# Kernel tuning notes

Hardware: AMD Instinct MI355X
Metric: run time of the kernel (lower is better)

Reference implementation:

```python
import jax, jax.numpy as jnp
import numpy as np

RANK = 8
ALPHA = 16.0
SCALING = ALPHA / RANK  # LoRA scaling alpha/rank
B, T, P, C = 8, 16, 197, 1024


def setup_inputs() -> dict:
    key = jax.random.key(0)
    k = jax.random.split(key, 8)
    hidden_states = jax.random.normal(k[0], (B, T, P, C), jnp.float32)
    frame_mask = jnp.ones((B, T), jnp.float32)
    # kaiming_uniform_(a=sqrt(5)) on an (out,in) Linear -> U(-1/sqrt(in), 1/sqrt(in))
    s_down = 1.0 / np.sqrt(C).astype(np.float32)
    down_w = jax.random.uniform(k[1], (RANK, C), jnp.float32, -s_down, s_down)
    # PyTorch LSTM default init: U(-1/sqrt(hidden), 1/sqrt(hidden)) for all params
    s_l = 1.0 / np.sqrt(RANK).astype(np.float32)
    w_ih = jax.random.uniform(k[2], (4 * RANK, RANK), jnp.float32, -s_l, s_l)
    w_hh = jax.random.uniform(k[3], (4 * RANK, RANK), jnp.float32, -s_l, s_l)
    b_ih = jax.random.uniform(k[4], (4 * RANK,), jnp.float32, -s_l, s_l)
    b_hh = jax.random.uniform(k[5], (4 * RANK,), jnp.float32, -s_l, s_l)
    # original zero-inits up; use small random so the reference output is non-trivial
    up_w = jax.random.normal(k[6], (C, RANK), jnp.float32) * 0.02
    return {
        "hidden_states": hidden_states,
        "num_frames": T,
        "frame_mask": frame_mask,
        "down_w": down_w,
        "w_ih": w_ih,
        "w_hh": w_hh,
        "b_ih": b_ih,
        "b_hh": b_hh,
        "up_w": up_w,
    }


def _lstm(x, w_ih, w_hh, b_ih, b_hh):
    """Single-layer unidirectional LSTM, PyTorch gate order (i,f,g,o).
    x: (T, N, R) time-major. Returns all hidden states (T, N, R)."""
    n, r = x.shape[1], w_hh.shape[1]
    bias = b_ih + b_hh

    def step(carry, x_t):
        h, c = carry
        gates = x_t @ w_ih.T + h @ w_hh.T + bias  # (N, 4R)
        i, f, g, o = jnp.split(gates, 4, axis=-1)
        c = jax.nn.sigmoid(f) * c + jax.nn.sigmoid(i) * jnp.tanh(g)
        h = jax.nn.sigmoid(o) * jnp.tanh(c)
        return (h, c), h

    init = (jnp.zeros((n, r), x.dtype), jnp.zeros((n, r), x.dtype))
    _, hs = jax.lax.scan(step, init, x)
    return hs


def reference(hidden_states, num_frames, frame_mask, down_w, w_ih, w_hh, b_ih, b_hh, up_w):
    b, t, p, c = hidden_states.shape
    assert t == num_frames
    # LoRA down: (B,T,P,C) x (R,C) -> (B,T,P,R)  (dropout is identity in eval)
    red = jnp.einsum('btpc,rc->btpr', hidden_states, down_w)
    red = red * frame_mask[:, :, None, None]
    # temporal LSTM over T, batch = B*P, in rank space
    seq = red.transpose(1, 0, 2, 3).reshape(t, b * p, -1)  # (T, B*P, R)
    hs = _lstm(seq, w_ih, w_hh, b_ih, b_hh)                # (T, B*P, R)
    out = hs.reshape(t, b, p, -1).transpose(1, 0, 2, 3)    # (B, T, P, R)
    out = out * frame_mask[:, :, None, None]
    # LoRA up + scaling: (B,T,P,R) x (C,R) -> (B,T,P,C)
    delta = jnp.einsum('btpr,or->btpo', out, up_w) * SCALING
    return delta
```

## Files before the change

kernel.cpp:

```cpp
#include <hip/hip_runtime.h>
#include <math.h>

#define BB 8
#define TT 16
#define PP 197
#define CC 1024
#define RR 8
#define NROWS (BB * TT * PP)
#define NPAIRS (NROWS / 2)
#define NSEQ  (BB * PP)
#define LORA_SCALE 2.0f

__device__ __forceinline__ float sigf(float x) {
    x = fminf(fmaxf(x, -30.f), 30.f);
    return 1.0f / (1.0f + __expf(-x));
}
__device__ __forceinline__ float tanh_fast(float x) {
    x = fminf(fmaxf(x, -15.f), 15.f);
    float e = __expf(-2.0f * x);
    return (1.0f - e) / (1.0f + e);
}
__device__ __forceinline__ float dot4(const float4& a, const float4& b) {
    return a.x * b.x + a.y * b.y + a.z * b.z + a.w * b.w;
}

__global__ __launch_bounds__(256) void k_down(const float* __restrict__ hs,
                                              const float* __restrict__ dw,
                                              const float* __restrict__ fm,
                                              float* __restrict__ red) {
    const int lane = threadIdx.x & 63;
    const int wid  = (blockIdx.x * blockDim.x + threadIdx.x) >> 6;
    const int nw   = (gridDim.x * blockDim.x) >> 6;

    float4 w[RR][4];
#pragma unroll
    for (int r = 0; r < RR; ++r)
#pragma unroll
        for (int k = 0; k < 4; ++k)
            w[r][k] = *(const float4*)(dw + r * CC + k * 256 + lane * 4);

    for (int pr = wid; pr < NPAIRS; pr += nw) {
        const int row0 = pr * 2;
        float4 xa[4], xb[4];
        const float* rpa = hs + (size_t)row0 * CC;
        const float* rpb = rpa + CC;
#pragma unroll
        for (int k = 0; k < 4; ++k) xa[k] = *(const float4*)(rpa + k * 256 + lane * 4);
#pragma unroll
        for (int k = 0; k < 4; ++k) xb[k] = *(const float4*)(rpb + k * 256 + lane * 4);

        float acca[RR], accb[RR];
#pragma unroll
        for (int r = 0; r < RR; ++r) {
            float a = 0.f, b = 0.f;
#pragma unroll
            for (int k = 0; k < 4; ++k) {
                a += dot4(xa[k], w[r][k]);
                b += dot4(xb[k], w[r][k]);
            }
            acca[r] = a; accb[r] = b;
        }
#pragma unroll
        for (int d = 32; d >= 1; d >>= 1) {
#pragma unroll
            for (int r = 0; r < RR; ++r) {
                acca[r] += __shfl_xor(acca[r], d, 64);
                accb[r] += __shfl_xor(accb[r], d, 64);
            }
        }
        if (lane == 0) {
            const float ma = fm[row0 / PP];
            const float mb = fm[(row0 + 1) / PP];
            float4* opa = (float4*)(red + (size_t)row0 * RR);
            opa[0] = make_float4(acca[0] * ma, acca[1] * ma, acca[2] * ma, acca[3] * ma);
            opa[1] = make_float4(acca[4] * ma, acca[5] * ma, acca[6] * ma, acca[7] * ma);
            opa[2] = make_float4(accb[0] * mb, accb[1] * mb, accb[2] * mb, accb[3] * mb);
            opa[3] = make_float4(accb[4] * mb, accb[5] * mb, accb[6] * mb, accb[7] * mb);
        }
    }
}

__global__ __launch_bounds__(64) void k_lstm(const float* __restrict__ red,
                                             const float* __restrict__ fm,
                                             const float* __restrict__ w_ih,
                                             const float* __restrict__ w_hh,
                                             const float* __restrict__ b_ih,
                                             const float* __restrict__ b_hh,
                                             float* __restrict__ hsm) {
    const int tid = blockIdx.x * blockDim.x + threadIdx.x;
    const int n = tid >> 3;
    const int r = tid & 7;
    const int lane = threadIdx.x & 63;
    const int grp = lane & 56;
    if (n >= NSEQ) return;

    float wi_i[8], wi_f[8], wi_g[8], wi_o[8];
    float wh_i[8], wh_f[8], wh_g[8], wh_o[8];
#pragma unroll
    for (int j = 0; j < 8; ++j) {
        wi_i[j] = w_ih[(r) * 8 + j];
        wi_f[j] = w_ih[(8 + r) * 8 + j];
        wi_g[j] = w_ih[(16 + r) * 8 + j];
        wi_o[j] = w_ih[(24 + r) * 8 + j];
        wh_i[j] = w_hh[(r) * 8 + j];
        wh_f[j] = w_hh[(8 + r) * 8 + j];
        wh_g[j] = w_hh[(16 + r) * 8 + j];
        wh_o[j] = w_hh[(24 + r) * 8 + j];
    }
    const float bi = b_ih[r] + b_hh[r];
    const float bf = b_ih[8 + r] + b_hh[8 + r];
    const float bg = b_ih[16 + r] + b_hh[16 + r];
    const float bo = b_ih[24 + r] + b_hh[24 + r];

    const int b = n / PP, p = n - (n / PP) * PP;
    const size_t base = ((size_t)b * TT * PP + p) * RR + r;
    const size_t tstride = (size_t)PP * RR;

    float xs[TT], msk[TT];
#pragma unroll
    for (int t = 0; t < TT; ++t) xs[t] = red[base + (size_t)t * tstride];
#pragma unroll
    for (int t = 0; t < TT; ++t) msk[t] = fm[b * TT + t];

    float h = 0.f, c = 0.f;
#pragma unroll
    for (int t = 0; t < TT; ++t) {
        float gi = bi, gf = bf, gg = bg, go = bo;
#pragma unroll
        for (int j = 0; j < 8; ++j) {
            const float xv = __shfl(xs[t], grp + j, 64);
            const float hv = __shfl(h, grp + j, 64);
            gi += wi_i[j] * xv + wh_i[j] * hv;
            gf += wi_f[j] * xv + wh_f[j] * hv;
            gg += wi_g[j] * xv + wh_g[j] * hv;
            go += wi_o[j] * xv + wh_o[j] * hv;
        }
        c = sigf(gf) * c + sigf(gi) * tanh_fast(gg);
        h = sigf(go) * tanh_fast(c);
        hsm[base + (size_t)t * tstride] = h * msk[t];
    }
}

__global__ __launch_bounds__(256) void k_up(const float* __restrict__ hsm,
                                            const float* __restrict__ up,
                                            float* __restrict__ out) {
    const int lane = threadIdx.x & 63;
    const int wid  = (blockIdx.x * blockDim.x + threadIdx.x) >> 6;
    const int nw   = (gridDim.x * blockDim.x) >> 6;

    float4 u0[16], u1[16];
#pragma unroll
    for (int g = 0; g < 16; ++g) {
        const float* pp = up + (size_t)(g * 64 + lane) * RR;
        u0[g] = *(const float4*)(pp);
        u1[g] = *(const float4*)(pp + 4);
    }

    for (int row = wid; row < NROWS; row += nw) {
        const float* hp = hsm + (size_t)row * RR;
        float4 h0 = *(const float4*)(hp);
        float4 h1 = *(const float4*)(hp + 4);
        h0.x *= LORA_SCALE; h0.y *= LORA_SCALE; h0.z *= LORA_SCALE; h0.w *= LORA_SCALE;
        h1.x *= LORA_SCALE; h1.y *= LORA_SCALE; h1.z *= LORA_SCALE; h1.w *= LORA_SCALE;
        float* op = out + (size_t)row * CC + lane;
#pragma unroll
        for (int g = 0; g < 16; ++g) {
            op[g * 64] = dot4(h0, u0[g]) + dot4(h1, u1[g]);
        }
    }
}

extern "C" void kernel_launch(void* const* d_in, const int* in_sizes, int n_in,
                              void* d_out, int out_size, void* d_ws, size_t ws_size,
                              hipStream_t stream) {
    const float* hs  = (const float*)d_in[0];
    const float* fm  = (const float*)d_in[2];
    const float* dw  = (const float*)d_in[3];
    const float* wih = (const float*)d_in[4];
    const float* whh = (const float*)d_in[5];
    const float* bih = (const float*)d_in[6];
    const float* bhh = (const float*)d_in[7];
    const float* up  = (const float*)d_in[8];
    float* out = (float*)d_out;

    float* red = (float*)d_ws;
    float* hsm = red + (size_t)NROWS * RR;

    k_down<<<512, 256, 0, stream>>>(hs, dw, fm, red);
    k_lstm<<<197, 64, 0, stream>>>(red, fm, wih, whh, bih, bhh, hsm);
    k_up<<<512, 256, 0, stream>>>(hsm, up, out);
}
```

Before: 210.6 us.

## Software-pipeline row loads in down/up kernels and double grid size

The down-projection kernel now handles one row per iteration and prefetches the next row's hidden states while computing the current one, replacing the previous two-rows-per-iteration batching. The up-projection kernel likewise prefetches the next row's rank vector. Both kernels gain a launch-bounds occupancy hint, and their grids double from 512 to 1024 blocks to put more waves in flight against the memory-bound streams. The prefetch costs extra registers, which may limit occupancy, and each row in k_down now pays its own full cross-lane reduction instead of sharing the shuffle loop across two rows.

```diff
diff --git a/kernel.cpp b/kernel.cpp
--- a/kernel.cpp
+++ b/kernel.cpp
@@ -7,7 +7,6 @@
 #define CC 1024
 #define RR 8
 #define NROWS (BB * TT * PP)
-#define NPAIRS (NROWS / 2)
 #define NSEQ  (BB * PP)
 #define LORA_SCALE 2.0f
 
@@ -24,10 +23,10 @@
     return a.x * b.x + a.y * b.y + a.z * b.z + a.w * b.w;
 }
 
-__global__ __launch_bounds__(256) void k_down(const float* __restrict__ hs,
-                                              const float* __restrict__ dw,
-                                              const float* __restrict__ fm,
-                                              float* __restrict__ red) {
+__global__ __launch_bounds__(256, 2) void k_down(const float* __restrict__ hs,
+                                                 const float* __restrict__ dw,
+                                                 const float* __restrict__ fm,
+                                                 float* __restrict__ red) {
     const int lane = threadIdx.x & 63;
     const int wid  = (blockIdx.x * blockDim.x + threadIdx.x) >> 6;
     const int nw   = (gridDim.x * blockDim.x) >> 6;
@@ -39,44 +38,49 @@
         for (int k = 0; k < 4; ++k)
             w[r][k] = *(const float4*)(dw + r * CC + k * 256 + lane * 4);
 
-    for (int pr = wid; pr < NPAIRS; pr += nw) {
-        const int row0 = pr * 2;
-        float4 xa[4], xb[4];
-        const float* rpa = hs + (size_t)row0 * CC;
-        const float* rpb = rpa + CC;
-#pragma unroll
-        for (int k = 0; k < 4; ++k) xa[k] = *(const float4*)(rpa + k * 256 + lane * 4);
-#pragma unroll
-        for (int k = 0; k < 4; ++k) xb[k] = *(const float4*)(rpb + k * 256 + lane * 4);
-
-        float acca[RR], accb[RR];
+    int row = wid;
+    if (row >= NROWS) return;
+
+    float4 xc[4];
+    {
+        const float* rp = hs + (size_t)row * CC;
+#pragma unroll
+        for (int k = 0; k < 4; ++k) xc[k] = *(const float4*)(rp + k * 256 + lane * 4);
+    }
+
+    while (true) {
+        const int nrow = row + nw;
+        const bool has_next = (nrow < NROWS);
+        float4 xn[4];
+        if (has_next) {
+            const float* rp = hs + (size_t)nrow * CC;
+#pragma unroll
+            for (int k = 0; k < 4; ++k) xn[k] = *(const float4*)(rp + k * 256 + lane * 4);
+        }
+
+        float acc[RR];
 #pragma unroll
         for (int r = 0; r < RR; ++r) {
-            float a = 0.f, b = 0.f;
-#pragma unroll
-            for (int k = 0; k < 4; ++k) {
-                a += dot4(xa[k], w[r][k]);
-                b += dot4(xb[k], w[r][k]);
-            }
-            acca[r] = a; accb[r] = b;
+            float a = 0.f;
+#pragma unroll
+            for (int k = 0; k < 4; ++k) a += dot4(xc[k], w[r][k]);
+            acc[r] = a;
         }
 #pragma unroll
         for (int d = 32; d >= 1; d >>= 1) {
 #pragma unroll
-            for (int r = 0; r < RR; ++r) {
-                acca[r] += __shfl_xor(acca[r], d, 64);
-                accb[r] += __shfl_xor(accb[r], d, 64);
-            }
+            for (int r = 0; r < RR; ++r) acc[r] += __shfl_xor(acc[r], d, 64);
         }
         if (lane == 0) {
-            const float ma = fm[row0 / PP];
-            const float mb = fm[(row0 + 1) / PP];
-            float4* opa = (float4*)(red + (size_t)row0 * RR);
-            opa[0] = make_float4(acca[0] * ma, acca[1] * ma, acca[2] * ma, acca[3] * ma);
-            opa[1] = make_float4(acca[4] * ma, acca[5] * ma, acca[6] * ma, acca[7] * ma);
-            opa[2] = make_float4(accb[0] * mb, accb[1] * mb, accb[2] * mb, accb[3] * mb);
-            opa[3] = make_float4(accb[4] * mb, accb[5] * mb, accb[6] * mb, accb[7] * mb);
-        }
+            const float m = fm[row / PP];
+            float4* op = (float4*)(red + (size_t)row * RR);
+            op[0] = make_float4(acc[0] * m, acc[1] * m, acc[2] * m, acc[3] * m);
+            op[1] = make_float4(acc[4] * m, acc[5] * m, acc[6] * m, acc[7] * m);
+        }
+        if (!has_next) break;
+        row = nrow;
+#pragma unroll
+        for (int k = 0; k < 4; ++k) xc[k] = xn[k];
     }
 }
 
@@ -141,9 +145,9 @@
     }
 }
 
-__global__ __launch_bounds__(256) void k_up(const float* __restrict__ hsm,
-                                            const float* __restrict__ up,
-                                            float* __restrict__ out) {
+__global__ __launch_bounds__(256, 2) void k_up(const float* __restrict__ hsm,
+                                               const float* __restrict__ up,
+                                               float* __restrict__ out) {
     const int lane = threadIdx.x & 63;
     const int wid  = (blockIdx.x * blockDim.x + threadIdx.x) >> 6;
     const int nw   = (gridDim.x * blockDim.x) >> 6;
@@ -156,10 +160,20 @@
         u1[g] = *(const float4*)(pp + 4);
     }
 
-    for (int row = wid; row < NROWS; row += nw) {
-        const float* hp = hsm + (size_t)row * RR;
-        float4 h0 = *(const float4*)(hp);
-        float4 h1 = *(const float4*)(hp + 4);
+    int row = wid;
+    if (row >= NROWS) return;
+
+    float4 h0 = *(const float4*)(hsm + (size_t)row * RR);
+    float4 h1 = *(const float4*)(hsm + (size_t)row * RR + 4);
+
+    while (true) {
+        const int nrow = row + nw;
+        const bool has_next = (nrow < NROWS);
+        float4 n0, n1;
+        if (has_next) {
+            n0 = *(const float4*)(hsm + (size_t)nrow * RR);
+            n1 = *(const float4*)(hsm + (size_t)nrow * RR + 4);
+        }
         h0.x *= LORA_SCALE; h0.y *= LORA_SCALE; h0.z *= LORA_SCALE; h0.w *= LORA_SCALE;
         h1.x *= LORA_SCALE; h1.y *= LORA_SCALE; h1.z *= LORA_SCALE; h1.w *= LORA_SCALE;
         float* op = out + (size_t)row * CC + lane;
@@ -167,6 +181,9 @@
         for (int g = 0; g < 16; ++g) {
             op[g * 64] = dot4(h0, u0[g]) + dot4(h1, u1[g]);
         }
+        if (!has_next) break;
+        row = nrow;
+        h0 = n0; h1 = n1;
     }
 }
 
@@ -186,7 +203,7 @@
     float* red = (float*)d_ws;
     float* hsm = red + (size_t)NROWS * RR;
 
-    k_down<<<512, 256, 0, stream>>>(hs, dw, fm, red);
+    k_down<<<1024, 256, 0, stream>>>(hs, dw, fm, red);
     k_lstm<<<197, 64, 0, stream>>>(red, fm, wih, whh, bih, bhh, hsm);
-    k_up<<<512, 256, 0, stream>>>(hsm, up, out);
-}
+    k_up<<<1024, 256, 0, stream>>>(hsm, up, out);
+}
```

After: 211.4 us. No clear change (+0.3%).

## Fuse down-projection, LSTM and up-projection into one per-sequence kernel

Applied to the files above, without the earlier changes.

Replaces the three-kernel pipeline with a single kernel where each 64-thread block owns one (batch, patch) sequence. The block computes all 16 down-projected rows with a 4-deep register prefetch, then runs the LSTM from shared memory and writes the up-projection directly. This removes the global round trips for the rank-8 intermediates and two kernel launches, and it takes the separate latency-bound LSTM kernel off the critical path. The cost is low occupancy: single-wave blocks with heavy register use, and serial phases inside each wave may limit memory-level parallelism.

```diff
diff --git a/kernel.cpp b/kernel.cpp
--- a/kernel.cpp
+++ b/kernel.cpp
@@ -6,8 +6,6 @@
 #define PP 197
 #define CC 1024
 #define RR 8
-#define NROWS (BB * TT * PP)
-#define NPAIRS (NROWS / 2)
 #define NSEQ  (BB * PP)
 #define LORA_SCALE 2.0f
 
@@ -24,148 +22,120 @@
     return a.x * b.x + a.y * b.y + a.z * b.z + a.w * b.w;
 }
 
-__global__ __launch_bounds__(256) void k_down(const float* __restrict__ hs,
-                                              const float* __restrict__ dw,
-                                              const float* __restrict__ fm,
-                                              float* __restrict__ red) {
-    const int lane = threadIdx.x & 63;
-    const int wid  = (blockIdx.x * blockDim.x + threadIdx.x) >> 6;
-    const int nw   = (gridDim.x * blockDim.x) >> 6;
+__global__ __launch_bounds__(64, 2) void k_fused(const float* __restrict__ hs,
+                                                 const float* __restrict__ fm,
+                                                 const float* __restrict__ dw,
+                                                 const float* __restrict__ w_ih,
+                                                 const float* __restrict__ w_hh,
+                                                 const float* __restrict__ b_ih,
+                                                 const float* __restrict__ b_hh,
+                                                 const float* __restrict__ up,
+                                                 float* __restrict__ out) {
+    __shared__ float red_lds[TT][RR];
+    __shared__ float h_lds[TT][RR];
 
-    float4 w[RR][4];
+    const int lane = threadIdx.x;
+    const int seq  = blockIdx.x;
+    const int b = seq / PP;
+    const int p = seq - b * PP;
+    const float* hsbase = hs + ((size_t)b * TT * PP + p) * CC;
+
+    {
+        float4 wreg[RR][4];
 #pragma unroll
-    for (int r = 0; r < RR; ++r)
+        for (int r = 0; r < RR; ++r)
 #pragma unroll
-        for (int k = 0; k < 4; ++k)
-            w[r][k] = *(const float4*)(dw + r * CC + k * 256 + lane * 4);
+            for (int k = 0; k < 4; ++k)
+                wreg[r][k] = *(const float4*)(dw + r * CC + k * 256 + lane * 4);
 
-    for (int pr = wid; pr < NPAIRS; pr += nw) {
-        const int row0 = pr * 2;
-        float4 xa[4], xb[4];
-        const float* rpa = hs + (size_t)row0 * CC;
-        const float* rpb = rpa + CC;
+        float4 buf[4][4];
 #pragma unroll
-        for (int k = 0; k < 4; ++k) xa[k] = *(const float4*)(rpa + k * 256 + lane * 4);
+        for (int t = 0; t < 4; ++t) {
+            const float* rp = hsbase + (size_t)t * PP * CC;
 #pragma unroll
-        for (int k = 0; k < 4; ++k) xb[k] = *(const float4*)(rpb + k * 256 + lane * 4);
-
-        float acca[RR], accb[RR];
-#pragma unroll
-        for (int r = 0; r < RR; ++r) {
-            float a = 0.f, b = 0.f;
-#pragma unroll
-            for (int k = 0; k < 4; ++k) {
-                a += dot4(xa[k], w[r][k]);
-                b += dot4(xb[k], w[r][k]);
-            }
-            acca[r] = a; accb[r] = b;
+            for (int k = 0; k < 4; ++k) buf[t][k] = *(const float4*)(rp + k * 256 + lane * 4);
         }
 #pragma unroll
-        for (int d = 32; d >= 1; d >>= 1) {
+        for (int t = 0; t < TT; ++t) {
+            const int s = t & 3;
+            float acc[RR];
 #pragma unroll
             for (int r = 0; r < RR; ++r) {
-                acca[r] += __shfl_xor(acca[r], d, 64);
-                accb[r] += __shfl_xor(accb[r], d, 64);
+                float a = 0.f;
+#pragma unroll
+                for (int k = 0; k < 4; ++k) a += dot4(buf[s][k], wreg[r][k]);
+                acc[r] = a;
+            }
+            if (t + 4 < TT) {
+                const float* rp = hsbase + (size_t)(t + 4) * PP * CC;
+#pragma unroll
+                for (int k = 0; k < 4; ++k) buf[s][k] = *(const float4*)(rp + k * 256 + lane * 4);
+            }
+#pragma unroll
+            for (int d = 32; d >= 1; d >>= 1)
+#pragma unroll
+                for (int r = 0; r < RR; ++r) acc[r] += __shfl_xor(acc[r], d, 64);
+            if (lane == 0) {
+                const float m = fm[b * TT + t];
+                *(float4*)&red_lds[t][0] = make_float4(acc[0] * m, acc[1] * m, acc[2] * m, acc[3] * m);
+                *(float4*)&red_lds[t][4] = make_float4(acc[4] * m, acc[5] * m, acc[6] * m, acc[7] * m);
             }
         }
-        if (lane == 0) {
-            const float ma = fm[row0 / PP];
-            const float mb = fm[(row0 + 1) / PP];
-            float4* opa = (float4*)(red + (size_t)row0 * RR);
-            opa[0] = make_float4(acca[0] * ma, acca[1] * ma, acca[2] * ma, acca[3] * ma);
-            opa[1] = make_float4(acca[4] * ma, acca[5] * ma, acca[6] * ma, acca[7] * ma);
-            opa[2] = make_float4(accb[0] * mb, accb[1] * mb, accb[2] * mb, accb[3] * mb);
-            opa[3] = make_float4(accb[4] * mb, accb[5] * mb, accb[6] * mb, accb[7] * mb);
+    }
+
+    {
+        const int r = lane & 7;
+        float wi[4][8], wh[4][8];
+#pragma unroll
+        for (int g = 0; g < 4; ++g)
+#pragma unroll
+            for (int j = 0; j < 8; ++j) {
+                wi[g][j] = w_ih[(g * 8 + r) * 8 + j];
+                wh[g][j] = w_hh[(g * 8 + r) * 8 + j];
+            }
+        const float bi = b_ih[r]      + b_hh[r];
+        const float bf = b_ih[8 + r]  + b_hh[8 + r];
+        const float bg = b_ih[16 + r] + b_hh[16 + r];
+        const float bo = b_ih[24 + r] + b_hh[24 + r];
+
+        float h = 0.f, c = 0.f;
+#pragma unroll
+        for (int t = 0; t < TT; ++t) {
+            const float4 x0 = *(const float4*)&red_lds[t][0];
+            const float4 x1 = *(const float4*)&red_lds[t][4];
+            float gi = bi, gf = bf, gg = bg, go = bo;
+            const float xs[8] = {x0.x, x0.y, x0.z, x0.w, x1.x, x1.y, x1.z, x1.w};
+#pragma unroll
+            for (int j = 0; j < 8; ++j) {
+                const float hv = __shfl(h, j, 64);
+                gi += wi[0][j] * xs[j] + wh[0][j] * hv;
+                gf += wi[1][j] * xs[j] + wh[1][j] * hv;
+                gg += wi[2][j] * xs[j] + wh[2][j] * hv;
+                go += wi[3][j] * xs[j] + wh[3][j] * hv;
+            }
+            c = sigf(gf) * c + sigf(gi) * tanh_fast(gg);
+            h = sigf(go) * tanh_fast(c);
+            if (lane < 8) h_lds[t][lane] = h * fm[b * TT + t] * LORA_SCALE;
         }
     }
-}
 
-__global__ __launch_bounds__(64) void k_lstm(const float* __restrict__ red,
-                                             const float* __restrict__ fm,
-                                             const float* __restrict__ w_ih,
-                                             const float* __restrict__ w_hh,
-                                             const float* __restrict__ b_ih,
-                                             const float* __restrict__ b_hh,
-                                             float* __restrict__ hsm) {
-    const int tid = blockIdx.x * blockDim.x + threadIdx.x;
-    const int n = tid >> 3;
-    const int r = tid & 7;
-    const int lane = threadIdx.x & 63;
-    const int grp = lane & 56;
-    if (n >= NSEQ) return;
-
-    float wi_i[8], wi_f[8], wi_g[8], wi_o[8];
-    float wh_i[8], wh_f[8], wh_g[8], wh_o[8];
-#pragma unroll
-    for (int j = 0; j < 8; ++j) {
-        wi_i[j] = w_ih[(r) * 8 + j];
-        wi_f[j] = w_ih[(8 + r) * 8 + j];
-        wi_g[j] = w_ih[(16 + r) * 8 + j];
-        wi_o[j] = w_ih[(24 + r) * 8 + j];
-        wh_i[j] = w_hh[(r) * 8 + j];
-        wh_f[j] = w_hh[(8 + r) * 8 + j];
-        wh_g[j] = w_hh[(16 + r) * 8 + j];
-        wh_o[j] = w_hh[(24 + r) * 8 + j];
-    }
-    const float bi = b_ih[r] + b_hh[r];
-    const float bf = b_ih[8 + r] + b_hh[8 + r];
-    const float bg = b_ih[16 + r] + b_hh[16 + r];
-    const float bo = b_ih[24 + r] + b_hh[24 + r];
-
-    const int b = n / PP, p = n - (n / PP) * PP;
-    const size_t base = ((size_t)b * TT * PP + p) * RR + r;
-    const size_t tstride = (size_t)PP * RR;
-
-    float xs[TT], msk[TT];
-#pragma unroll
-    for (int t = 0; t < TT; ++t) xs[t] = red[base + (size_t)t * tstride];
-#pragma unroll
-    for (int t = 0; t < TT; ++t) msk[t] = fm[b * TT + t];
-
-    float h = 0.f, c = 0.f;
-#pragma unroll
-    for (int t = 0; t < TT; ++t) {
-        float gi = bi, gf = bf, gg = bg, go = bo;
-#pragma unroll
-        for (int j = 0; j < 8; ++j) {
-            const float xv = __shfl(xs[t], grp + j, 64);
-            const float hv = __shfl(h, grp + j, 64);
-            gi += wi_i[j] * xv + wh_i[j] * hv;
-            gf += wi_f[j] * xv + wh_f[j] * hv;
-            gg += wi_g[j] * xv + wh_g[j] * hv;
-            go += wi_o[j] * xv + wh_o[j] * hv;
-        }
-        c = sigf(gf) * c + sigf(gi) * tanh_fast(gg);
-        h = sigf(go) * tanh_fast(c);
-        hsm[base + (size_t)t * tstride] = h * msk[t];
-    }
-}
-
-__global__ __launch_bounds__(256) void k_up(const float* __restrict__ hsm,
-                                            const float* __restrict__ up,
-                                            float* __restrict__ out) {
-    const int lane = threadIdx.x & 63;
-    const int wid  = (blockIdx.x * blockDim.x + threadIdx.x) >> 6;
-    const int nw   = (gridDim.x * blockDim.x) >> 6;
-
-    float4 u0[16], u1[16];
-#pragma unroll
-    for (int g = 0; g < 16; ++g) {
-        const float* pp = up + (size_t)(g * 64 + lane) * RR;
-        u0[g] = *(const float4*)(pp);
-        u1[g] = *(const float4*)(pp + 4);
-    }
-
-    for (int row = wid; row < NROWS; row += nw) {
-        const float* hp = hsm + (size_t)row * RR;
-        float4 h0 = *(const float4*)(hp);
-        float4 h1 = *(const float4*)(hp + 4);
-        h0.x *= LORA_SCALE; h0.y *= LORA_SCALE; h0.z *= LORA_SCALE; h0.w *= LORA_SCALE;
-        h1.x *= LORA_SCALE; h1.y *= LORA_SCALE; h1.z *= LORA_SCALE; h1.w *= LORA_SCALE;
-        float* op = out + (size_t)row * CC + lane;
+    {
+        float4 u0[16], u1[16];
 #pragma unroll
         for (int g = 0; g < 16; ++g) {
-            op[g * 64] = dot4(h0, u0[g]) + dot4(h1, u1[g]);
+            const float* pp = up + (size_t)(g * 64 + lane) * RR;
+            u0[g] = *(const float4*)(pp);
+            u1[g] = *(const float4*)(pp + 4);
+        }
+        float* obase = out + ((size_t)b * TT * PP + p) * CC + lane;
+#pragma unroll
+        for (int t = 0; t < TT; ++t) {
+            const float4 h0 = *(const float4*)&h_lds[t][0];
+            const float4 h1 = *(const float4*)&h_lds[t][4];
+            float* op = obase + (size_t)t * PP * CC;
+#pragma unroll
+            for (int g = 0; g < 16; ++g)
+                op[g * 64] = dot4(h0, u0[g]) + dot4(h1, u1[g]);
         }
     }
 }
@@ -183,10 +153,5 @@
     const float* up  = (const float*)d_in[8];
     float* out = (float*)d_out;
 
-    float* red = (float*)d_ws;
-    float* hsm = red + (size_t)NROWS * RR;
-
-    k_down<<<512, 256, 0, stream>>>(hs, dw, fm, red);
-    k_lstm<<<197, 64, 0, stream>>>(red, fm, wih, whh, bih, bhh, hsm);
-    k_up<<<512, 256, 0, stream>>>(hsm, up, out);
+    k_fused<<<NSEQ, 64, 0, stream>>>(hs, fm, dw, wih, whh, bih, bhh, up, out);
 }
```

After: 208.5 us. About the same (-1.0%).
